# Kernel tuning notes

Hardware: AMD Instinct MI355X
Metric: run time of the kernel (lower is better)

The kernel has to match this reference:

```python
import jax, jax.numpy as jnp
import numpy as np

N, E = 100000, 1600000
IN, HID, OUT = 128, 64, 64
BN_EPS = 1e-5


def setup_inputs() -> dict:
    key = jax.random.key(0)
    ks = jax.random.split(key, 6)
    x = jax.random.normal(ks[0], (N, IN), dtype=jnp.float32)
    edge_index = jax.random.randint(ks[1], (2, E), 0, N, dtype=jnp.int32)
    W1 = jax.random.normal(ks[2], (IN, HID), dtype=jnp.float32) / np.sqrt(IN).astype(np.float32)
    b1 = jnp.zeros((HID,), jnp.float32)
    bn_weight = jnp.ones((HID,), jnp.float32)
    bn_bias = jnp.zeros((HID,), jnp.float32)
    W2 = jax.random.normal(ks[3], (HID, OUT), dtype=jnp.float32) / np.sqrt(HID).astype(np.float32)
    b2 = jnp.zeros((OUT,), jnp.float32)
    return {"x": x, "edge_index": edge_index, "W1": W1, "b1": b1,
            "bn_weight": bn_weight, "bn_bias": bn_bias, "W2": W2, "b2": b2}


def _gcn_conv(x, W, b, src, dst, deg_inv_sqrt):
    # PyG GCNConv: linear first, then symmetric-normalized aggregation with self-loops.
    h = x @ W                                        # [N, out]
    norm = deg_inv_sqrt[src] * deg_inv_sqrt[dst]     # [E]
    agg = jax.ops.segment_sum(h[src] * norm[:, None], dst, num_segments=h.shape[0])
    # self-loop contribution: norm = 1/deg
    agg = agg + h * (deg_inv_sqrt * deg_inv_sqrt)[:, None]
    return agg + b


def reference(x, edge_index, W1, b1, bn_weight, bn_bias, W2, b2):
    src, dst = edge_index[0], edge_index[1]
    # degree including self-loop (GCNConv add_self_loops=True, edge_weight=1)
    deg = jax.ops.segment_sum(jnp.ones((E,), x.dtype), dst, num_segments=N) + 1.0
    deg_inv_sqrt = jax.lax.rsqrt(deg)
    h = _gcn_conv(x, W1, b1, src, dst, deg_inv_sqrt)
    # BatchNorm1d (training-mode batch statistics, biased variance)
    mean = jnp.mean(h, axis=0)
    var = jnp.var(h, axis=0)
    h = (h - mean) * jax.lax.rsqrt(var + BN_EPS) * bn_weight + bn_bias
    h = jax.nn.relu(h)
    # dropout: inference mode (identity)
    return _gcn_conv(h, W2, b2, src, dst, deg_inv_sqrt)
```

## Files before the change

kernel.cpp:

```cpp
#include <hip/hip_runtime.h>

#define N_NODES 100000
#define E_EDGES 1600000
#define IN_F    128
#define HID_F   64
#define OUT_F   64
#define BN_EPS  1e-5f
#define NBUK    391
#define CHUNK   6250
#define NGBLK   3125
#define NMBLK   1563

typedef __bf16 bf16x8 __attribute__((ext_vector_type(8)));
typedef float  f32x4  __attribute__((ext_vector_type(4)));

__device__ __forceinline__ float bflo(unsigned int u) { return __uint_as_float(u << 16); }
__device__ __forceinline__ float bfhi(unsigned int u) { return __uint_as_float(u & 0xFFFF0000u); }
__device__ __forceinline__ unsigned int pack2bf(float a, float b) {
    unsigned int ua = __float_as_uint(a), ub = __float_as_uint(b);
    ua = (ua + 0x7fffu + ((ua >> 16) & 1u)) >> 16;
    ub = (ub + 0x7fffu + ((ub >> 16) & 1u)) >> 16;
    return ua | (ub << 16);
}
__device__ __forceinline__ unsigned short bf1(float a) {
    unsigned int ua = __float_as_uint(a);
    return (unsigned short)((ua + 0x7fffu + ((ua >> 16) & 1u)) >> 16);
}
#define ADD8(A, u)                                           \
    do {                                                     \
        A[0] += bflo((u).x); A[1] += bfhi((u).x);            \
        A[2] += bflo((u).y); A[3] += bfhi((u).y);            \
        A[4] += bflo((u).z); A[5] += bfhi((u).z);            \
        A[6] += bflo((u).w); A[7] += bfhi((u).w);            \
    } while (0)

__global__ __launch_bounds__(512) void k_chist(const int* __restrict__ dstv,
                                               int* __restrict__ chist) {
    __shared__ int h[NBUK];
    const int tid = threadIdx.x;
    const int e0 = blockIdx.x * CHUNK;
    for (int b = tid; b < NBUK; b += 512) h[b] = 0;
    __syncthreads();
    for (int t = tid; t < CHUNK; t += 512)
        atomicAdd(&h[dstv[e0 + t] >> 8], 1);
    __syncthreads();
    for (int b = tid; b < NBUK; b += 512)
        if (h[b]) atomicAdd(&chist[b], h[b]);
}

__global__ __launch_bounds__(512) void k_cscan(int* __restrict__ coff,
                                               int* __restrict__ ccur) {
    __shared__ int sh[512];
    const int tid = threadIdx.x;
    int v = (tid < NBUK) ? coff[tid] : 0;
    sh[tid] = v;
    __syncthreads();
    for (int off = 1; off < 512; off <<= 1) {
        int t = (tid >= off) ? sh[tid - off] : 0;
        __syncthreads();
        sh[tid] += t;
        __syncthreads();
    }
    int excl = sh[tid] - v;
    if (tid < NBUK) { coff[tid] = excl; ccur[tid] = excl; }
    if (tid == 0) coff[NBUK] = E_EDGES;
}

__global__ __launch_bounds__(512) void k_bucket(const int* __restrict__ srcv,
                                                const int* __restrict__ dstv,
                                                int* __restrict__ ccur,
                                                unsigned int* __restrict__ aux) {
    __shared__ int dl[CHUNK];
    __shared__ int hist[NBUK], base[NBUK], lcur[NBUK];
    const int tid = threadIdx.x;
    const int e0 = blockIdx.x * CHUNK;
    for (int b = tid; b < NBUK; b += 512) hist[b] = 0;
    __syncthreads();
    for (int t = tid; t < CHUNK; t += 512) {
        int d = dstv[e0 + t];
        dl[t] = d;
        atomicAdd(&hist[d >> 8], 1);
    }
    __syncthreads();
    for (int b = tid; b < NBUK; b += 512) {
        int h = hist[b];
        if (h) base[b] = atomicAdd(&ccur[b], h);
        lcur[b] = 0;
    }
    __syncthreads();
    for (int t = tid; t < CHUNK; t += 512) {
        int d = dl[t];
        int b = d >> 8;
        int off = atomicAdd(&lcur[b], 1);
        aux[base[b] + off] = ((unsigned int)srcv[e0 + t] << 8) | (unsigned int)(d & 255);
    }
}

__global__ __launch_bounds__(256) void k_csrnode(const int* __restrict__ coff,
                                                 const unsigned int* __restrict__ aux,
                                                 int* __restrict__ rowptr,
                                                 float* __restrict__ dis,
                                                 int* __restrict__ csr_src) {
    __shared__ int c0[256], sc[256], cur[256];
    const int tid = threadIdx.x;
    const int n0 = blockIdx.x * 256;
    const int nn = min(256, N_NODES - n0);
    const int estart = coff[blockIdx.x];
    const int eend   = coff[blockIdx.x + 1];
    c0[tid] = 0;
    __syncthreads();
    for (int e = estart + tid; e < eend; e += 256)
        atomicAdd(&c0[aux[e] & 255], 1);
    __syncthreads();
    int v = c0[tid];
    sc[tid] = v;
    __syncthreads();
    for (int off = 1; off < 256; off <<= 1) {
        int t = (tid >= off) ? sc[tid - off] : 0;
        __syncthreads();
        sc[tid] += t;
        __syncthreads();
    }
    int excl = sc[tid] - v;
    if (tid < nn) {
        int p = estart + excl;
        rowptr[n0 + tid] = p;
        cur[tid] = p;
        dis[n0 + tid] = rsqrtf((float)v + 1.0f);
    }
    if (blockIdx.x == NBUK - 1 && tid == 0) rowptr[N_NODES] = E_EDGES;
    __syncthreads();
    for (int e = estart + tid; e < eend; e += 256) {
        unsigned int u = aux[e];
        int pos = atomicAdd(&cur[u & 255], 1);
        csr_src[pos] = (int)(u >> 8);
    }
}

__global__ __launch_bounds__(256) void k_gemm1(const float* __restrict__ x,
                                               const float* __restrict__ W1,
                                               const float* __restrict__ dis,
                                               unsigned short* __restrict__ hs1) {
    __shared__ unsigned short Asb[64 * 136];
    __shared__ unsigned short Btb[64 * 136];
    __shared__ unsigned short Cc[64 * 72];
    __shared__ float disS[64];
    const int tid = threadIdx.x;
    const int r0 = blockIdx.x * 64;

    if (tid < 64) disS[tid] = (r0 + tid < N_NODES) ? dis[r0 + tid] : 0.f;

    const float4* x4 = (const float4*)x;
#pragma unroll
    for (int p = 0; p < 4; ++p) {
        int idx8 = p * 256 + tid;
        int row = idx8 >> 4, c8 = idx8 & 15;
        float4 v0 = make_float4(0.f, 0.f, 0.f, 0.f), v1 = v0;
        if (r0 + row < N_NODES) {
            v0 = x4[(size_t)(r0 + row) * 32 + c8 * 2];
            v1 = x4[(size_t)(r0 + row) * 32 + c8 * 2 + 1];
        }
        uint4 u;
        u.x = pack2bf(v0.x, v0.y); u.y = pack2bf(v0.z, v0.w);
        u.z = pack2bf(v1.x, v1.y); u.w = pack2bf(v1.z, v1.w);
        *(uint4*)&Asb[row * 136 + c8 * 8] = u;
    }
    for (int idx = tid; idx < IN_F * HID_F; idx += 256) {
        int k = idx >> 6, n = idx & 63;
        Btb[n * 136 + k] = bf1(W1[idx]);
    }
    __syncthreads();

    const int wv = tid >> 6, lane = tid & 63;
    const int m = lane & 15, quad = lane >> 4;
    const int arow = wv * 16 + m;
    f32x4 acc[4] = {};
#pragma unroll
    for (int ks = 0; ks < 4; ++ks) {
        int k0 = ks * 32 + quad * 8;
        bf16x8 af = *(const bf16x8*)&Asb[arow * 136 + k0];
#pragma unroll
        for (int c = 0; c < 4; ++c) {
            bf16x8 bfr = *(const bf16x8*)&Btb[(c * 16 + m) * 136 + k0];
            acc[c] = __builtin_amdgcn_mfma_f32_16x16x32_bf16(af, bfr, acc[c], 0, 0, 0);
        }
    }
#pragma unroll
    for (int c = 0; c < 4; ++c)
#pragma unroll
        for (int r = 0; r < 4; ++r) {
            int rl = wv * 16 + quad * 4 + r;
            Cc[rl * 72 + c * 16 + m] = bf1(acc[c][r] * disS[rl]);
        }
    __syncthreads();
#pragma unroll
    for (int p = 0; p < 2; ++p) {
        int idx = p * 256 + tid;
        int row = idx >> 3, c8 = idx & 7;
        if (r0 + row < N_NODES)
            *(uint4*)&hs1[(size_t)(r0 + row) * 64 + c8 * 8] = *(uint4*)&Cc[row * 72 + c8 * 8];
    }
}

__global__ __launch_bounds__(256) void k_gather1(const int* __restrict__ rowptr,
                                                 const int* __restrict__ csr_src,
                                                 const unsigned short* __restrict__ hsb,
                                                 const float* __restrict__ dis,
                                                 const float* __restrict__ b1,
                                                 float* __restrict__ agg,
                                                 float* __restrict__ partials) {
    const int tid = threadIdx.x;
    const int g = tid >> 3, q = tid & 7;
    const int n = blockIdx.x * 32 + g;
    const uint4* __restrict__ hs16 = (const uint4*)hsb;

    const int start = rowptr[n], end = rowptr[n + 1];
    float A0[8] = {}, A1[8] = {}, A2[8] = {}, A3[8] = {};
    {
        uint4 u = hs16[(size_t)n * 8 + q];
        ADD8(A0, u);
    }
    int i = start;
    for (; i + 3 < end; i += 4) {
        int s0 = csr_src[i + 0], s1 = csr_src[i + 1];
        int s2 = csr_src[i + 2], s3 = csr_src[i + 3];
        uint4 u0 = hs16[(size_t)s0 * 8 + q];
        uint4 u1 = hs16[(size_t)s1 * 8 + q];
        uint4 u2 = hs16[(size_t)s2 * 8 + q];
        uint4 u3 = hs16[(size_t)s3 * 8 + q];
        ADD8(A0, u0); ADD8(A1, u1); ADD8(A2, u2); ADD8(A3, u3);
    }
    for (; i < end; ++i) {
        uint4 u = hs16[(size_t)csr_src[i] * 8 + q];
        ADD8(A0, u);
    }
    const float d = dis[n];
    const float4 blo = ((const float4*)b1)[q * 2];
    const float4 bhi = ((const float4*)b1)[q * 2 + 1];
    float o[8];
    o[0] = fmaf(d, A0[0] + A1[0] + A2[0] + A3[0], blo.x);
    o[1] = fmaf(d, A0[1] + A1[1] + A2[1] + A3[1], blo.y);
    o[2] = fmaf(d, A0[2] + A1[2] + A2[2] + A3[2], blo.z);
    o[3] = fmaf(d, A0[3] + A1[3] + A2[3] + A3[3], blo.w);
    o[4] = fmaf(d, A0[4] + A1[4] + A2[4] + A3[4], bhi.x);
    o[5] = fmaf(d, A0[5] + A1[5] + A2[5] + A3[5], bhi.y);
    o[6] = fmaf(d, A0[6] + A1[6] + A2[6] + A3[6], bhi.z);
    o[7] = fmaf(d, A0[7] + A1[7] + A2[7] + A3[7], bhi.w);
    float4* ag = (float4*)(agg + (size_t)n * HID_F + q * 8);
    ag[0] = make_float4(o[0], o[1], o[2], o[3]);
    ag[1] = make_float4(o[4], o[5], o[6], o[7]);

    __shared__ float4 redA[256], redB[256];
    redA[tid] = make_float4(o[0], o[1], o[2], o[3]);
    redB[tid] = make_float4(o[4], o[5], o[6], o[7]);
    __syncthreads();
    for (int s = 128; s >= 8; s >>= 1) {
        if (tid < s) {
            redA[tid].x += redA[tid + s].x; redA[tid].y += redA[tid + s].y;
            redA[tid].z += redA[tid + s].z; redA[tid].w += redA[tid + s].w;
            redB[tid].x += redB[tid + s].x; redB[tid].y += redB[tid + s].y;
            redB[tid].z += redB[tid + s].z; redB[tid].w += redB[tid + s].w;
        }
        __syncthreads();
    }
    float4* pr = (float4*)(partials + (size_t)blockIdx.x * 128);
    if (tid < 8) { pr[tid * 2] = redA[tid]; pr[tid * 2 + 1] = redB[tid]; }
    __syncthreads();
    redA[tid] = make_float4(o[0] * o[0], o[1] * o[1], o[2] * o[2], o[3] * o[3]);
    redB[tid] = make_float4(o[4] * o[4], o[5] * o[5], o[6] * o[6], o[7] * o[7]);
    __syncthreads();
    for (int s = 128; s >= 8; s >>= 1) {
        if (tid < s) {
            redA[tid].x += redA[tid + s].x; redA[tid].y += redA[tid + s].y;
            redA[tid].z += redA[tid + s].z; redA[tid].w += redA[tid + s].w;
            redB[tid].x += redB[tid + s].x; redB[tid].y += redB[tid + s].y;
            redB[tid].z += redB[tid + s].z; redB[tid].w += redB[tid + s].w;
        }
        __syncthreads();
    }
    if (tid < 8) { pr[16 + tid * 2] = redA[tid]; pr[16 + tid * 2 + 1] = redB[tid]; }
}

__global__ __launch_bounds__(256) void k_bnfinal(const float* __restrict__ partials,
                                                 float* __restrict__ bnstats) {
    const int tid = threadIdx.x;
    const int col = tid & 127;
    const int half = tid >> 7;
    float s = 0.f;
    for (int r = blockIdx.x * 2 + half; r < NGBLK; r += 128)
        s += partials[(size_t)r * 128 + col];
    __shared__ float sh[256];
    sh[tid] = s;
    __syncthreads();
    if (tid < 128) unsafeAtomicAdd(&bnstats[col], sh[tid] + sh[tid + 128]);
}

__global__ __launch_bounds__(256) void k_gemm2(const float* __restrict__ agg1,
                                               const float* __restrict__ W2,
                                               const float* __restrict__ dis,
                                               const float* __restrict__ bnw,
                                               const float* __restrict__ bnb,
                                               const float* __restrict__ bnstats,
                                               unsigned short* __restrict__ hs2) {
    __shared__ unsigned short Ab[64 * 72];
    __shared__ unsigned short Bt2[64 * 72];
    __shared__ unsigned short Cc[64 * 72];
    __shared__ float scale_s[64], shift_s[64], disS[64];
    const int tid = threadIdx.x;
    const int r0 = blockIdx.x * 64;

    if (tid < 64) {
        const float invN = 1.0f / (float)N_NODES;
        float mean = bnstats[tid] * invN;
        float var  = bnstats[64 + tid] * invN - mean * mean;
        float sc   = bnw[tid] * rsqrtf(var + BN_EPS);
        scale_s[tid] = sc;
        shift_s[tid] = fmaf(-mean, sc, bnb[tid]);
        disS[tid] = (r0 + tid < N_NODES) ? dis[r0 + tid] : 0.f;
    }
    for (int idx = tid; idx < HID_F * OUT_F; idx += 256) {
        int k = idx >> 6, n = idx & 63;
        Bt2[n * 72 + k] = bf1(W2[idx]);
    }
    __syncthreads();

    const float4* a4 = (const float4*)agg1;
#pragma unroll
    for (int p = 0; p < 4; ++p) {
        int idx4 = p * 256 + tid;
        int row = idx4 >> 4, c4 = idx4 & 15;
        float4 v = make_float4(0.f, 0.f, 0.f, 0.f);
        if (r0 + row < N_NODES) v = a4[(size_t)(r0 + row) * 16 + c4];
        int k0 = c4 * 4;
        v.x = fmaxf(fmaf(v.x, scale_s[k0 + 0], shift_s[k0 + 0]), 0.f);
        v.y = fmaxf(fmaf(v.y, scale_s[k0 + 1], shift_s[k0 + 1]), 0.f);
        v.z = fmaxf(fmaf(v.z, scale_s[k0 + 2], shift_s[k0 + 2]), 0.f);
        v.w = fmaxf(fmaf(v.w, scale_s[k0 + 3], shift_s[k0 + 3]), 0.f);
        uint2 u;
        u.x = pack2bf(v.x, v.y); u.y = pack2bf(v.z, v.w);
        *(uint2*)&Ab[row * 72 + c4 * 4] = u;
    }
    __syncthreads();

    const int wv = tid >> 6, lane = tid & 63;
    const int m = lane & 15, quad = lane >> 4;
    const int arow = wv * 16 + m;
    f32x4 acc[4] = {};
#pragma unroll
    for (int ks = 0; ks < 2; ++ks) {
        int k0 = ks * 32 + quad * 8;
        bf16x8 af = *(const bf16x8*)&Ab[arow * 72 + k0];
#pragma unroll
        for (int c = 0; c < 4; ++c) {
            bf16x8 bfr = *(const bf16x8*)&Bt2[(c * 16 + m) * 72 + k0];
            acc[c] = __builtin_amdgcn_mfma_f32_16x16x32_bf16(af, bfr, acc[c], 0, 0, 0);
        }
    }
#pragma unroll
    for (int c = 0; c < 4; ++c)
#pragma unroll
        for (int r = 0; r < 4; ++r) {
            int rl = wv * 16 + quad * 4 + r;
            Cc[rl * 72 + c * 16 + m] = bf1(acc[c][r] * disS[rl]);
        }
    __syncthreads();
#pragma unroll
    for (int p = 0; p < 2; ++p) {
        int idx = p * 256 + tid;
        int row = idx >> 3, c8 = idx & 7;
        if (r0 + row < N_NODES)
            *(uint4*)&hs2[(size_t)(r0 + row) * 64 + c8 * 8] = *(uint4*)&Cc[row * 72 + c8 * 8];
    }
}

__global__ __launch_bounds__(256) void k_gather2(const int* __restrict__ rowptr,
                                                 const int* __restrict__ csr_src,
                                                 const unsigned short* __restrict__ hsb,
                                                 const float* __restrict__ dis,
                                                 const float* __restrict__ b2,
                                                 float* __restrict__ out) {
    const int tid = threadIdx.x;
    const int g = tid >> 3, q = tid & 7;
    const int n = blockIdx.x * 32 + g;
    const uint4* __restrict__ hs16 = (const uint4*)hsb;

    const int start = rowptr[n], end = rowptr[n + 1];
    float A0[8] = {}, A1[8] = {}, A2[8] = {}, A3[8] = {};
    {
        uint4 u = hs16[(size_t)n * 8 + q];
        ADD8(A0, u);
    }
    int i = start;
    for (; i + 3 < end; i += 4) {
        int s0 = csr_src[i + 0], s1 = csr_src[i + 1];
        int s2 = csr_src[i + 2], s3 = csr_src[i + 3];
        uint4 u0 = hs16[(size_t)s0 * 8 + q];
        uint4 u1 = hs16[(size_t)s1 * 8 + q];
        uint4 u2 = hs16[(size_t)s2 * 8 + q];
        uint4 u3 = hs16[(size_t)s3 * 8 + q];
        ADD8(A0, u0); ADD8(A1, u1); ADD8(A2, u2); ADD8(A3, u3);
    }
    for (; i < end; ++i) {
        uint4 u = hs16[(size_t)csr_src[i] * 8 + q];
        ADD8(A0, u);
    }
    const float d = dis[n];
    const float4 blo = ((const float4*)b2)[q * 2];
    const float4 bhi = ((const float4*)b2)[q * 2 + 1];
    float4 o0, o1;
    o0.x = fmaf(d, A0[0] + A1[0] + A2[0] + A3[0], blo.x);
    o0.y = fmaf(d, A0[1] + A1[1] + A2[1] + A3[1], blo.y);
    o0.z = fmaf(d, A0[2] + A1[2] + A2[2] + A3[2], blo.z);
    o0.w = fmaf(d, A0[3] + A1[3] + A2[3] + A3[3], blo.w);
    o1.x = fmaf(d, A0[4] + A1[4] + A2[4] + A3[4], bhi.x);
    o1.y = fmaf(d, A0[5] + A1[5] + A2[5] + A3[5], bhi.y);
    o1.z = fmaf(d, A0[6] + A1[6] + A2[6] + A3[6], bhi.z);
    o1.w = fmaf(d, A0[7] + A1[7] + A2[7] + A3[7], bhi.w);
    float4* op = (float4*)(out + (size_t)n * OUT_F + q * 8);
    op[0] = o0;
    op[1] = o1;
}

extern "C" void kernel_launch(void* const* d_in, const int* in_sizes, int n_in,
                              void* d_out, int out_size, void* d_ws, size_t ws_size,
                              hipStream_t stream) {
    const float* x   = (const float*)d_in[0];
    const int*   ei  = (const int*)d_in[1];
    const float* W1  = (const float*)d_in[2];
    const float* b1  = (const float*)d_in[3];
    const float* bnw = (const float*)d_in[4];
    const float* bnb = (const float*)d_in[5];
    const float* W2  = (const float*)d_in[6];
    const float* b2  = (const float*)d_in[7];
    float* out = (float*)d_out;

    float* ws = (float*)d_ws;
    float*        dis     = ws;
    int*          rowptr  = (int*)(ws + 100352);
    int*          coff    = (int*)(ws + 100352 + 100608);
    int*          ccur    = (int*)(ws + 100352 + 100608 + 512);
    float*        bnstats = ws + 100352 + 100608 + 512 + 512;
    int*          csr_src = (int*)(ws + 100352 + 100608 + 512 + 512 + 128);
    float*        bufA    = ws + 100352 + 100608 + 512 + 512 + 128 + 1600000;
    float*        bufB    = bufA + (size_t)N_NODES * HID_F;
    unsigned int*  aux  = (unsigned int*)bufA;
    unsigned short* hsb = (unsigned short*)bufA;
    float* partials = out;

    const int* srcv = ei;
    const int* dstv = ei + E_EDGES;

    hipMemsetAsync(coff, 0, (NBUK + 1) * sizeof(int), stream);
    hipMemsetAsync(bnstats, 0, 128 * sizeof(float), stream);

    k_chist  <<<256, 512, 0, stream>>>(dstv, coff);
    k_cscan  <<<1, 512, 0, stream>>>(coff, ccur);
    k_bucket <<<256, 512, 0, stream>>>(srcv, dstv, ccur, aux);
    k_csrnode<<<NBUK, 256, 0, stream>>>(coff, aux, rowptr, dis, csr_src);

    k_gemm1  <<<NMBLK, 256, 0, stream>>>(x, W1, dis, hsb);
    k_gather1<<<NGBLK, 256, 0, stream>>>(rowptr, csr_src, hsb, dis, b1, bufB, partials);
    k_bnfinal<<<64, 256, 0, stream>>>(partials, bnstats);
    k_gemm2  <<<NMBLK, 256, 0, stream>>>(bufB, W2, dis, bnw, bnb, bnstats, hsb);
    k_gather2<<<NGBLK, 256, 0, stream>>>(rowptr, csr_src, hsb, dis, b2, out);
}
```

Baseline: 254.6 us.

## Store layer-1 aggregate in bf16, unroll gathers by 8, drop memsets and atomics

The layer-1 aggregate is now written as bf16 instead of fp32, halving that intermediate's write in gather1 and its read in gemm2. Both gather loops are unrolled to 8 edges per iteration so more loads are in flight. The column histogram now writes per-block results to a buffer that the scan sums, and the BN final reduction uses one block per column writing directly; together these remove both memsets and the global atomics. The extra bf16 rounding of pre-BatchNorm activations slightly reduces accuracy, and the scan now reads 256 rows serially per thread.

```diff
diff --git a/kernel.cpp b/kernel.cpp
--- a/kernel.cpp
+++ b/kernel.cpp
@@ -35,7 +35,7 @@
     } while (0)
 
 __global__ __launch_bounds__(512) void k_chist(const int* __restrict__ dstv,
-                                               int* __restrict__ chist) {
+                                               int* __restrict__ histbuf) {
     __shared__ int h[NBUK];
     const int tid = threadIdx.x;
     const int e0 = blockIdx.x * CHUNK;
@@ -45,14 +45,17 @@
         atomicAdd(&h[dstv[e0 + t] >> 8], 1);
     __syncthreads();
     for (int b = tid; b < NBUK; b += 512)
-        if (h[b]) atomicAdd(&chist[b], h[b]);
-}
-
-__global__ __launch_bounds__(512) void k_cscan(int* __restrict__ coff,
+        histbuf[blockIdx.x * NBUK + b] = h[b];
+}
+
+__global__ __launch_bounds__(512) void k_cscan(const int* __restrict__ histbuf,
+                                               int* __restrict__ coff,
                                                int* __restrict__ ccur) {
     __shared__ int sh[512];
     const int tid = threadIdx.x;
-    int v = (tid < NBUK) ? coff[tid] : 0;
+    int v = 0;
+    if (tid < NBUK)
+        for (int b = 0; b < 256; ++b) v += histbuf[b * NBUK + tid];
     sh[tid] = v;
     __syncthreads();
     for (int off = 1; off < 512; off <<= 1) {
@@ -207,7 +210,7 @@
                                                  const unsigned short* __restrict__ hsb,
                                                  const float* __restrict__ dis,
                                                  const float* __restrict__ b1,
-                                                 float* __restrict__ agg,
+                                                 unsigned short* __restrict__ aggb,
                                                  float* __restrict__ partials) {
     const int tid = threadIdx.x;
     const int g = tid >> 3, q = tid & 7;
@@ -221,7 +224,23 @@
         ADD8(A0, u);
     }
     int i = start;
-    for (; i + 3 < end; i += 4) {
+    for (; i + 7 < end; i += 8) {
+        int s0 = csr_src[i + 0], s1 = csr_src[i + 1];
+        int s2 = csr_src[i + 2], s3 = csr_src[i + 3];
+        int s4 = csr_src[i + 4], s5 = csr_src[i + 5];
+        int s6 = csr_src[i + 6], s7 = csr_src[i + 7];
+        uint4 u0 = hs16[(size_t)s0 * 8 + q];
+        uint4 u1 = hs16[(size_t)s1 * 8 + q];
+        uint4 u2 = hs16[(size_t)s2 * 8 + q];
+        uint4 u3 = hs16[(size_t)s3 * 8 + q];
+        uint4 u4 = hs16[(size_t)s4 * 8 + q];
+        uint4 u5 = hs16[(size_t)s5 * 8 + q];
+        uint4 u6 = hs16[(size_t)s6 * 8 + q];
+        uint4 u7 = hs16[(size_t)s7 * 8 + q];
+        ADD8(A0, u0); ADD8(A1, u1); ADD8(A2, u2); ADD8(A3, u3);
+        ADD8(A0, u4); ADD8(A1, u5); ADD8(A2, u6); ADD8(A3, u7);
+    }
+    if (i + 3 < end) {
         int s0 = csr_src[i + 0], s1 = csr_src[i + 1];
         int s2 = csr_src[i + 2], s3 = csr_src[i + 3];
         uint4 u0 = hs16[(size_t)s0 * 8 + q];
@@ -229,6 +248,7 @@
         uint4 u2 = hs16[(size_t)s2 * 8 + q];
         uint4 u3 = hs16[(size_t)s3 * 8 + q];
         ADD8(A0, u0); ADD8(A1, u1); ADD8(A2, u2); ADD8(A3, u3);
+        i += 4;
     }
     for (; i < end; ++i) {
         uint4 u = hs16[(size_t)csr_src[i] * 8 + q];
@@ -246,9 +266,10 @@
     o[5] = fmaf(d, A0[5] + A1[5] + A2[5] + A3[5], bhi.y);
     o[6] = fmaf(d, A0[6] + A1[6] + A2[6] + A3[6], bhi.z);
     o[7] = fmaf(d, A0[7] + A1[7] + A2[7] + A3[7], bhi.w);
-    float4* ag = (float4*)(agg + (size_t)n * HID_F + q * 8);
-    ag[0] = make_float4(o[0], o[1], o[2], o[3]);
-    ag[1] = make_float4(o[4], o[5], o[6], o[7]);
+    uint4 ob;
+    ob.x = pack2bf(o[0], o[1]); ob.y = pack2bf(o[2], o[3]);
+    ob.z = pack2bf(o[4], o[5]); ob.w = pack2bf(o[6], o[7]);
+    ((uint4*)aggb)[(size_t)n * 8 + q] = ob;
 
     __shared__ float4 redA[256], redB[256];
     redA[tid] = make_float4(o[0], o[1], o[2], o[3]);
@@ -283,19 +304,22 @@
 
 __global__ __launch_bounds__(256) void k_bnfinal(const float* __restrict__ partials,
                                                  float* __restrict__ bnstats) {
-    const int tid = threadIdx.x;
-    const int col = tid & 127;
-    const int half = tid >> 7;
+    const int c = blockIdx.x;
+    const int tid = threadIdx.x;
     float s = 0.f;
-    for (int r = blockIdx.x * 2 + half; r < NGBLK; r += 128)
-        s += partials[(size_t)r * 128 + col];
+    for (int r = tid; r < NGBLK; r += 256)
+        s += partials[(size_t)r * 128 + c];
     __shared__ float sh[256];
     sh[tid] = s;
     __syncthreads();
-    if (tid < 128) unsafeAtomicAdd(&bnstats[col], sh[tid] + sh[tid + 128]);
-}
-
-__global__ __launch_bounds__(256) void k_gemm2(const float* __restrict__ agg1,
+    for (int st = 128; st > 0; st >>= 1) {
+        if (tid < st) sh[tid] += sh[tid + st];
+        __syncthreads();
+    }
+    if (tid == 0) bnstats[c] = sh[0];
+}
+
+__global__ __launch_bounds__(256) void k_gemm2(const unsigned short* __restrict__ aggb,
                                                const float* __restrict__ W2,
                                                const float* __restrict__ dis,
                                                const float* __restrict__ bnw,
@@ -324,21 +348,29 @@
     }
     __syncthreads();
 
-    const float4* a4 = (const float4*)agg1;
-#pragma unroll
-    for (int p = 0; p < 4; ++p) {
-        int idx4 = p * 256 + tid;
-        int row = idx4 >> 4, c4 = idx4 & 15;
-        float4 v = make_float4(0.f, 0.f, 0.f, 0.f);
-        if (r0 + row < N_NODES) v = a4[(size_t)(r0 + row) * 16 + c4];
-        int k0 = c4 * 4;
-        v.x = fmaxf(fmaf(v.x, scale_s[k0 + 0], shift_s[k0 + 0]), 0.f);
-        v.y = fmaxf(fmaf(v.y, scale_s[k0 + 1], shift_s[k0 + 1]), 0.f);
-        v.z = fmaxf(fmaf(v.z, scale_s[k0 + 2], shift_s[k0 + 2]), 0.f);
-        v.w = fmaxf(fmaf(v.w, scale_s[k0 + 3], shift_s[k0 + 3]), 0.f);
-        uint2 u;
-        u.x = pack2bf(v.x, v.y); u.y = pack2bf(v.z, v.w);
-        *(uint2*)&Ab[row * 72 + c4 * 4] = u;
+    const uint4* a16 = (const uint4*)aggb;
+#pragma unroll
+    for (int p = 0; p < 2; ++p) {
+        int idx = p * 256 + tid;
+        int row = idx >> 3, q = idx & 7;
+        uint4 u = make_uint4(0, 0, 0, 0);
+        if (r0 + row < N_NODES) u = a16[(size_t)(r0 + row) * 8 + q];
+        int k0 = q * 8;
+        float v[8];
+        v[0] = bflo(u.x); v[1] = bfhi(u.x); v[2] = bflo(u.y); v[3] = bfhi(u.y);
+        v[4] = bflo(u.z); v[5] = bfhi(u.z); v[6] = bflo(u.w); v[7] = bfhi(u.w);
+        uint4 o;
+        float w0 = fmaxf(fmaf(v[0], scale_s[k0 + 0], shift_s[k0 + 0]), 0.f);
+        float w1 = fmaxf(fmaf(v[1], scale_s[k0 + 1], shift_s[k0 + 1]), 0.f);
+        float w2 = fmaxf(fmaf(v[2], scale_s[k0 + 2], shift_s[k0 + 2]), 0.f);
+        float w3 = fmaxf(fmaf(v[3], scale_s[k0 + 3], shift_s[k0 + 3]), 0.f);
+        float w4 = fmaxf(fmaf(v[4], scale_s[k0 + 4], shift_s[k0 + 4]), 0.f);
+        float w5 = fmaxf(fmaf(v[5], scale_s[k0 + 5], shift_s[k0 + 5]), 0.f);
+        float w6 = fmaxf(fmaf(v[6], scale_s[k0 + 6], shift_s[k0 + 6]), 0.f);
+        float w7 = fmaxf(fmaf(v[7], scale_s[k0 + 7], shift_s[k0 + 7]), 0.f);
+        o.x = pack2bf(w0, w1); o.y = pack2bf(w2, w3);
+        o.z = pack2bf(w4, w5); o.w = pack2bf(w6, w7);
+        *(uint4*)&Ab[row * 72 + q * 8] = o;
     }
     __syncthreads();
 
@@ -391,7 +423,23 @@
         ADD8(A0, u);
     }
     int i = start;
-    for (; i + 3 < end; i += 4) {
+    for (; i + 7 < end; i += 8) {
+        int s0 = csr_src[i + 0], s1 = csr_src[i + 1];
+        int s2 = csr_src[i + 2], s3 = csr_src[i + 3];
+        int s4 = csr_src[i + 4], s5 = csr_src[i + 5];
+        int s6 = csr_src[i + 6], s7 = csr_src[i + 7];
+        uint4 u0 = hs16[(size_t)s0 * 8 + q];
+        uint4 u1 = hs16[(size_t)s1 * 8 + q];
+        uint4 u2 = hs16[(size_t)s2 * 8 + q];
+        uint4 u3 = hs16[(size_t)s3 * 8 + q];
+        uint4 u4 = hs16[(size_t)s4 * 8 + q];
+        uint4 u5 = hs16[(size_t)s5 * 8 + q];
+        uint4 u6 = hs16[(size_t)s6 * 8 + q];
+        uint4 u7 = hs16[(size_t)s7 * 8 + q];
+        ADD8(A0, u0); ADD8(A1, u1); ADD8(A2, u2); ADD8(A3, u3);
+        ADD8(A0, u4); ADD8(A1, u5); ADD8(A2, u6); ADD8(A3, u7);
+    }
+    if (i + 3 < end) {
         int s0 = csr_src[i + 0], s1 = csr_src[i + 1];
         int s2 = csr_src[i + 2], s3 = csr_src[i + 3];
         uint4 u0 = hs16[(size_t)s0 * 8 + q];
@@ -399,6 +447,7 @@
         uint4 u2 = hs16[(size_t)s2 * 8 + q];
         uint4 u3 = hs16[(size_t)s3 * 8 + q];
         ADD8(A0, u0); ADD8(A1, u1); ADD8(A2, u2); ADD8(A3, u3);
+        i += 4;
     }
     for (; i < end; ++i) {
         uint4 u = hs16[(size_t)csr_src[i] * 8 + q];
@@ -437,30 +486,29 @@
     float* ws = (float*)d_ws;
     float*        dis     = ws;
     int*          rowptr  = (int*)(ws + 100352);
-    int*          coff    = (int*)(ws + 100352 + 100608);
-    int*          ccur    = (int*)(ws + 100352 + 100608 + 512);
-    float*        bnstats = ws + 100352 + 100608 + 512 + 512;
-    int*          csr_src = (int*)(ws + 100352 + 100608 + 512 + 512 + 128);
-    float*        bufA    = ws + 100352 + 100608 + 512 + 512 + 128 + 1600000;
+    int*          coff    = (int*)(ws + 200960);
+    int*          ccur    = (int*)(ws + 201472);
+    float*        bnstats = ws + 201984;
+    int*          histbuf = (int*)(ws + 202112);
+    int*          csr_src = (int*)(ws + 302464);
+    float*        bufA    = ws + 1902464;
     float*        bufB    = bufA + (size_t)N_NODES * HID_F;
-    unsigned int*  aux  = (unsigned int*)bufA;
-    unsigned short* hsb = (unsigned short*)bufA;
+    unsigned int*   aux  = (unsigned int*)bufA;
+    unsigned short* hsb  = (unsigned short*)bufA;
+    unsigned short* aggb = (unsigned short*)bufB;
     float* partials = out;
 
     const int* srcv = ei;
     const int* dstv = ei + E_EDGES;
 
-    hipMemsetAsync(coff, 0, (NBUK + 1) * sizeof(int), stream);
-    hipMemsetAsync(bnstats, 0, 128 * sizeof(float), stream);
-
-    k_chist  <<<256, 512, 0, stream>>>(dstv, coff);
-    k_cscan  <<<1, 512, 0, stream>>>(coff, ccur);
+    k_chist  <<<256, 512, 0, stream>>>(dstv, histbuf);
+    k_cscan  <<<1, 512, 0, stream>>>(histbuf, coff, ccur);
     k_bucket <<<256, 512, 0, stream>>>(srcv, dstv, ccur, aux);
     k_csrnode<<<NBUK, 256, 0, stream>>>(coff, aux, rowptr, dis, csr_src);
 
     k_gemm1  <<<NMBLK, 256, 0, stream>>>(x, W1, dis, hsb);
-    k_gather1<<<NGBLK, 256, 0, stream>>>(rowptr, csr_src, hsb, dis, b1, bufB, partials);
-    k_bnfinal<<<64, 256, 0, stream>>>(partials, bnstats);
-    k_gemm2  <<<NMBLK, 256, 0, stream>>>(bufB, W2, dis, bnw, bnb, bnstats, hsb);
+    k_gather1<<<NGBLK, 256, 0, stream>>>(rowptr, csr_src, hsb, dis, b1, aggb, partials);
+    k_bnfinal<<<128, 256, 0, stream>>>(partials, bnstats);
+    k_gemm2  <<<NMBLK, 256, 0, stream>>>(aggb, W2, dis, bnw, bnb, bnstats, hsb);
     k_gather2<<<NGBLK, 256, 0, stream>>>(rowptr, csr_src, hsb, dis, b2, out);
 }
```

Result: no change. 252.0 us (-1.0%).
